# Performance work log

Measured on AMD Instinct MI355X. Metric: run time of the kernel, lower is better.

## Reference

```python
import jax, jax.numpy as jnp
import numpy as np

B, S, H = 2, 2048, 768
NH, DH = 12, 64  # num_heads, dim_head; inner_dim = NH*DH = H
SCALE = DH ** -0.5


def setup_inputs() -> dict:
    key = jax.random.key(0)
    k1, k2, k3 = jax.random.split(key, 3)
    x = jax.random.normal(k1, (B, S, H), dtype=jnp.float32)
    w_qkv = jax.random.normal(k2, (3 * NH * DH, H), dtype=jnp.float32) * (H ** -0.5)
    w_out = jax.random.normal(k3, (H, NH * DH), dtype=jnp.float32) * ((NH * DH) ** -0.5)
    b_out = jnp.zeros((H,), dtype=jnp.float32)
    return {"x": x, "w_qkv": w_qkv, "w_out": w_out, "b_out": b_out}


def reference(x, w_qkv, w_out, b_out):
    b, s, _ = x.shape
    # qkv linear: [b, s, 3*inner]
    qkv = jnp.einsum('bsh,oh->bso', x, w_qkv)
    # 'b s (qkv l d) -> qkv b l s d'  (l = heads)
    qkv = qkv.reshape(b, s, 3, NH, DH).transpose(2, 0, 3, 1, 4)
    q, k, v = qkv[0], qkv[1], qkv[2]  # each [b, nh, s, dh]
    att = jax.nn.softmax(jnp.einsum('bhxd,bhyd->bhxy', q, k) * SCALE, axis=-1)
    out = jnp.einsum('bhxy,bhyd->bhxd', att, v)  # [b, nh, s, dh]
    out = out.transpose(0, 2, 1, 3).reshape(b, s, NH * DH)  # 'b h l d -> b l (h d)'
    return jnp.einsum('bsi,oi->bso', out, w_out) + b_out
```

## Files before the change

### kernel.cpp

```cpp
#include <hip/hip_runtime.h>
#include <cstdint>
#include <cstddef>

typedef __bf16 bf16;
typedef __bf16 bf16x8 __attribute__((ext_vector_type(8)));
typedef __bf16 bf16x4 __attribute__((ext_vector_type(4)));
typedef float  f32x4  __attribute__((ext_vector_type(4)));
typedef float  f32x16 __attribute__((ext_vector_type(16)));

constexpr int Bb  = 2;
constexpr int Ss  = 2048;
constexpr int Hh  = 768;
constexpr int NHh = 12;
constexpr int DHh = 64;
constexpr int Mm  = Bb * Ss;
constexpr int N3  = 3 * Hh;
constexpr int QKW = 2 * Hh;

__device__ __forceinline__ float fexp2(float x) { return __builtin_amdgcn_exp2f(x); }

__device__ __forceinline__ void gload_lds16(void* lds, const void* g) {
  __builtin_amdgcn_global_load_lds(
      (__attribute__((address_space(1))) void*)(uintptr_t)g,
      (__attribute__((address_space(3))) void*)(uint32_t)(uintptr_t)lds,
      16, 0, 0);
}

__device__ __forceinline__ void cfence() { asm volatile("" ::: "memory"); }

__global__ void cvt3_f32_bf16(const float* __restrict__ x,  bf16* __restrict__ xb,
                              const float* __restrict__ w1, bf16* __restrict__ w1b,
                              const float* __restrict__ w2, bf16* __restrict__ w2b) {
  const int st = gridDim.x * blockDim.x;
  int i0 = blockIdx.x * blockDim.x + threadIdx.x;
  for (int i = i0; i < 786432; i += st) {
    float4 v = ((const float4*)x)[i];
    bf16x4 o; o[0]=(bf16)v.x; o[1]=(bf16)v.y; o[2]=(bf16)v.z; o[3]=(bf16)v.w;
    ((bf16x4*)xb)[i] = o;
  }
  for (int i = i0; i < 442368; i += st) {
    float4 v = ((const float4*)w1)[i];
    bf16x4 o; o[0]=(bf16)v.x; o[1]=(bf16)v.y; o[2]=(bf16)v.z; o[3]=(bf16)v.w;
    ((bf16x4*)w1b)[i] = o;
  }
  for (int i = i0; i < 147456; i += st) {
    float4 v = ((const float4*)w2)[i];
    bf16x4 o; o[0]=(bf16)v.x; o[1]=(bf16)v.y; o[2]=(bf16)v.z; o[3]=(bf16)v.w;
    ((bf16x4*)w2b)[i] = o;
  }
}

template<int CSTRIDE, int OUTMODE, int BM>
__global__ __launch_bounds__(256, 2)
void gemm_bt(const bf16* __restrict__ A, const bf16* __restrict__ Bw,
             bf16* __restrict__ Cb, bf16* __restrict__ VtG,
             float* __restrict__ Cf, const float* __restrict__ bias)
{
  constexpr int K = 768;
  constexpr int NT = K / 32;
  constexpr int MI = BM / 32;
  constexpr int ABUF = BM * 64;
  __shared__ bf16 As[2][BM * 32];
  __shared__ bf16 Bs[2][128 * 32];
  const int tid  = threadIdx.x;
  const int wid  = tid >> 6, lane = tid & 63;
  const int lr   = lane & 15, lk = lane >> 4;
  const int n0   = blockIdx.x * 128, m0 = blockIdx.y * BM;
  const int wm   = (wid >> 1) * (BM / 2), wn = (wid & 1) * 64;

  f32x4 acc[MI][4] = {};

  const char* Ag = (const char*)(A  + (size_t)m0 * K) + (size_t)(tid >> 2) * (K * 2) + (tid & 3) * 16;
  const char* Bg = (const char*)(Bw + (size_t)n0 * K) + (size_t)(tid >> 2) * (K * 2) + (tid & 3) * 16;
  constexpr size_t rstep = (size_t)64 * K * 2;

  auto stage = [&](int buf, int kb) {
    char* aw = (char*)As + buf * ABUF + wid * 1024;
    char* bw = (char*)Bs + buf * 8192 + wid * 1024;
    gload_lds16(aw, Ag + (size_t)kb * 2);
    if constexpr (BM == 128)
      gload_lds16(aw + 4096, Ag + rstep + (size_t)kb * 2);
    gload_lds16(bw,        Bg + (size_t)kb * 2);
    gload_lds16(bw + 4096, Bg + rstep + (size_t)kb * 2);
  };

  stage(0, 0);
  asm volatile("s_waitcnt vmcnt(0)" ::: "memory");
  __syncthreads();

#pragma unroll 1
  for (int t = 0; t < NT; ++t) {
    const int cur = t & 1;
    if (t + 1 < NT) stage(cur ^ 1, (t + 1) * 32);
    __builtin_amdgcn_sched_barrier(0);

    bf16x8 af[MI], bfv[4];
#pragma unroll
    for (int i = 0; i < MI; ++i)
      af[i]  = *(const bf16x8*)((const char*)As + cur * ABUF + ((wm + i * 16 + lr) * 32 + lk * 8) * 2);
#pragma unroll
    for (int j = 0; j < 4; ++j)
      bfv[j] = *(const bf16x8*)((const char*)Bs + cur * 8192 + ((wn + j * 16 + lr) * 32 + lk * 8) * 2);
#pragma unroll
    for (int i = 0; i < MI; ++i)
#pragma unroll
      for (int j = 0; j < 4; ++j)
        acc[i][j] = __builtin_amdgcn_mfma_f32_16x16x32_bf16(af[i], bfv[j], acc[i][j], 0, 0, 0);

    __syncthreads();
  }

  if constexpr (OUTMODE == 1) {
#pragma unroll
    for (int i = 0; i < MI; ++i)
#pragma unroll
      for (int j = 0; j < 4; ++j) {
        const int n = n0 + wn + j * 16 + lr;
        const float bv = bias[n];
#pragma unroll
        for (int r = 0; r < 4; ++r) {
          const int m = m0 + wm + i * 16 + lk * 4 + r;
          Cf[(size_t)m * CSTRIDE + n] = acc[i][j][r] + bv;
        }
      }
  } else {
    if (n0 < QKW) {
#pragma unroll
      for (int i = 0; i < MI; ++i)
#pragma unroll
        for (int j = 0; j < 4; ++j) {
          const int n = n0 + wn + j * 16 + lr;
#pragma unroll
          for (int r = 0; r < 4; ++r) {
            const int m = m0 + wm + i * 16 + lk * 4 + r;
            Cb[(size_t)m * CSTRIDE + n] = (bf16)acc[i][j][r];
          }
        }
    } else {
      const int bidx = m0 >> 11;
      const int s0 = (m0 & 2047) + wm + lk * 4;
#pragma unroll
      for (int i = 0; i < MI; ++i)
#pragma unroll
        for (int j = 0; j < 4; ++j) {
          const int colv = (n0 - QKW) + wn + j * 16 + lr;
          const int hh = colv >> 6, dd = colv & 63;
          const int bh = bidx * NHh + hh;
          const int mb = s0 + i * 16;
          bf16x4 pv;
#pragma unroll
          for (int r = 0; r < 4; ++r) pv[r] = (bf16)acc[i][j][r];
          const size_t idx8 = (((size_t)bh * 128 + (mb >> 4)) * 2 + (dd >> 5)) * 64
                              + ((mb >> 3) & 1) * 32 + (dd & 31);
          *(bf16x4*)(VtG + idx8 * 8 + (mb & 7)) = pv;
        }
    }
  }
}

__global__ __launch_bounds__(256, 3)
void attn_fwd5(const bf16* __restrict__ qk, const bf16* __restrict__ Vfrag,
               bf16* __restrict__ aout)
{
  __shared__ __align__(16) char lds[32768];
  const int tid  = threadIdx.x;
  const int wid  = tid >> 6, lane = tid & 63;
  const int lq   = lane & 31, hi = lane >> 5;
  const int qh   = wid & 1, grp = wid >> 1;

  const int orig = blockIdx.x;
  const int swz  = (orig & 7) * 96 + (orig >> 3);
  const int qb   = swz & 31;
  const int bh   = swz >> 5;
  const int b    = bh / NHh, h = bh % NHh;
  const int q0   = qb * 64 + qh * 32;
  const int kvbase = grp * 1024;

  constexpr float Cs = 0.18033688011112042f;
  const bf16* qrow = qk + (size_t)(b * Ss + q0 + lq) * QKW + h * DHh;
  bf16x8 qf[4];
#pragma unroll
  for (int j = 0; j < 4; ++j) {
    bf16x8 t = *(const bf16x8*)(qrow + j * 16 + hi * 8);
#pragma unroll
    for (int e = 0; e < 8; ++e) t[e] = (bf16)((float)t[e] * Cs);
    qf[j] = t;
  }

  const int strow = qh * 32 + (lane >> 3);
  const int stcol = ((lane & 7) * 16) ^ (((lane >> 3) & 7) << 4);
  const char* Kg0 = (const char*)(qk + (size_t)(b * Ss) * QKW + Hh + h * DHh)
                    + (size_t)strow * (QKW * 2) + stcol;
  auto stageK = [&](int buf, int kvt) {
    char* db = lds + grp * 16384 + buf * 8192 + qh * 4096;
    const char* sg = Kg0 + (size_t)kvt * (QKW * 2);
#pragma unroll
    for (int c = 0; c < 4; ++c)
      gload_lds16(db + c * 1024, sg + (size_t)(c * 8) * (QKW * 2));
  };

  const char* Vf = (const char*)Vfrag + (size_t)bh * 262144 + lane * 16;

  f32x16 oacc[2] = {};
  f32x16 lacc = {};
  bf16x8 ones;
#pragma unroll
  for (int e = 0; e < 8; ++e) ones[e] = (bf16)1.0f;

  stageK(0, kvbase);
  asm volatile("s_waitcnt vmcnt(0)" ::: "memory");
  __builtin_amdgcn_sched_barrier(0);

#pragma unroll 1
  for (int i = 0; i < 16; ++i) {
    const int cur = i & 1;

    cfence();
    __builtin_amdgcn_s_barrier();
    cfence();

    bf16x8 vf[4][2];
    {
      const char* vp = Vf + (size_t)(grp * 64 + i * 4) * 2048;
#pragma unroll
      for (int s = 0; s < 4; ++s)
#pragma unroll
        for (int dc = 0; dc < 2; ++dc)
          vf[s][dc] = *(const bf16x8*)(vp + (s * 2 + dc) * 1024);
    }

    stageK(cur ^ 1, kvbase + ((i + 1) & 15) * 64);
    __builtin_amdgcn_sched_barrier(0);

    f32x16 sacc[2];
    __builtin_amdgcn_s_setprio(1);
#pragma unroll
    for (int kvc = 0; kvc < 2; ++kvc) {
      f32x16 s = {};
      const int row = kvc * 32 + lq;
      const char* kb = lds + grp * 16384 + cur * 8192 + row * 128;
      const int sw = (lq & 7) << 4;
#pragma unroll
      for (int j = 0; j < 4; ++j) {
        bf16x8 kf = *(const bf16x8*)(kb + ((j * 32 + hi * 16) ^ sw));
        s = __builtin_amdgcn_mfma_f32_32x32x16_bf16(kf, qf[j], s, 0, 0, 0);
      }
      sacc[kvc] = s;
    }
    __builtin_amdgcn_s_setprio(0);

    uint32_t w[2][8];
#pragma unroll
    for (int kvc = 0; kvc < 2; ++kvc)
#pragma unroll
      for (int m = 0; m < 8; ++m) {
        union { bf16 hh[2]; uint32_t u; } cv;
        cv.hh[0] = (bf16)fexp2(sacc[kvc][2 * m]);
        cv.hh[1] = (bf16)fexp2(sacc[kvc][2 * m + 1]);
        w[kvc][m] = cv.u;
      }

    asm volatile("s_waitcnt vmcnt(4)" ::: "memory");
    __builtin_amdgcn_sched_barrier(0);

    __builtin_amdgcn_s_setprio(1);
#pragma unroll
    for (int s = 0; s < 4; ++s) {
      const int kvc = s >> 1, sb = s & 1;
      uint32_t a0 = w[kvc][4 * sb + 0], b0 = w[kvc][4 * sb + 2];
      uint32_t a1 = w[kvc][4 * sb + 1], b1 = w[kvc][4 * sb + 3];
      asm("v_permlane32_swap_b32 %0, %1" : "+v"(a0), "+v"(b0));
      asm("v_permlane32_swap_b32 %0, %1" : "+v"(a1), "+v"(b1));
      union { uint32_t u[4]; bf16x8 v; } pf;
      pf.u[0] = a0; pf.u[1] = a1; pf.u[2] = b0; pf.u[3] = b1;
#pragma unroll
      for (int dc = 0; dc < 2; ++dc)
        oacc[dc] = __builtin_amdgcn_mfma_f32_32x32x16_bf16(vf[s][dc], pf.v, oacc[dc], 0, 0, 0);
      lacc = __builtin_amdgcn_mfma_f32_32x32x16_bf16(ones, pf.v, lacc, 0, 0, 0);
    }
    __builtin_amdgcn_s_setprio(0);

    asm volatile("s_waitcnt vmcnt(0)" ::: "memory");
    __builtin_amdgcn_sched_barrier(0);
  }

  __syncthreads();

  if (grp == 1) {
    char* mb = lds + qh * 8704;
#pragma unroll
    for (int dc = 0; dc < 2; ++dc)
#pragma unroll
      for (int rr = 0; rr < 4; ++rr) {
        f32x4 t;
#pragma unroll
        for (int e = 0; e < 4; ++e) t[e] = oacc[dc][rr * 4 + e];
        *(f32x4*)(mb + (dc * 4 + rr) * 1024 + lane * 16) = t;
      }
    *(float*)(mb + 8192 + lane * 4) = lacc[0];
  }
  __syncthreads();
  if (grp == 0) {
    const char* mb = lds + qh * 8704;
    const float l2 = *(const float*)(mb + 8192 + lane * 4);
    const float linv = 1.0f / (lacc[0] + l2);
    bf16* orow = aout + (size_t)(b * Ss + q0 + lq) * Hh + h * DHh;
#pragma unroll
    for (int dc = 0; dc < 2; ++dc)
#pragma unroll
      for (int rr = 0; rr < 4; ++rr) {
        const f32x4 o2 = *(const f32x4*)(mb + (dc * 4 + rr) * 1024 + lane * 16);
        bf16x4 ov;
#pragma unroll
        for (int e = 0; e < 4; ++e)
          ov[e] = (bf16)((oacc[dc][rr * 4 + e] + o2[e]) * linv);
        *(bf16x4*)(orow + dc * 32 + rr * 8 + hi * 4) = ov;
      }
  }
}

extern "C" void kernel_launch(void* const* d_in, const int* in_sizes, int n_in,
                              void* d_out, int out_size, void* d_ws, size_t ws_size,
                              hipStream_t stream) {
  const float* x     = (const float*)d_in[0];
  const float* w_qkv = (const float*)d_in[1];
  const float* w_out = (const float*)d_in[2];
  const float* b_out = (const float*)d_in[3];
  char* ws = (char*)d_ws;
  bf16* xb    = (bf16*)(ws + 0);
  bf16* wqkvb = (bf16*)(ws + 6291456);
  bf16* woutb = (bf16*)(ws + 9830400);
  bf16* qkb   = (bf16*)(ws + 11010048);
  bf16* Vfrag = (bf16*)(ws + 23592960);
  bf16* aoutb = (bf16*)(ws + 29884416);

  cvt3_f32_bf16<<<2048, 256, 0, stream>>>(x, xb, w_qkv, wqkvb, w_out, woutb);

  gemm_bt<QKW, 0, 128><<<dim3(18, 32), 256, 0, stream>>>(xb, wqkvb, qkb, Vfrag, nullptr, nullptr);
  attn_fwd5<<<768, 256, 0, stream>>>(qkb, Vfrag, aoutb);
  gemm_bt<Hh, 1, 64><<<dim3(6, 64), 256, 0, stream>>>(aoutb, woutb, nullptr, nullptr,
                                                      (float*)d_out, b_out);
}
```

Before: 87.76 us.

## Write K in MFMA fragment layout from QKV GEMM for contiguous attention staging

The QKV projection epilogue now writes Q to its own row-major buffer and writes K directly in a per-head, MFMA-fragment-ordered layout, as was already done for V. The attention kernel then stages K tiles with fully contiguous 16-byte global-to-LDS loads and reads them from LDS without the XOR swizzle. The intended gains are coalesced K loads and conflict-free LDS reads in the attention loop. The cost is scattered 2-byte scalar stores in the GEMM epilogue for K, which may slow the projection kernel.

```diff
diff --git a/kernel.cpp b/kernel.cpp
--- a/kernel.cpp
+++ b/kernel.cpp
@@ -50,10 +50,10 @@
   }
 }
 
-template<int CSTRIDE, int OUTMODE, int BM>
+template<int OUTMODE, int BM>
 __global__ __launch_bounds__(256, 2)
 void gemm_bt(const bf16* __restrict__ A, const bf16* __restrict__ Bw,
-             bf16* __restrict__ Cb, bf16* __restrict__ VtG,
+             bf16* __restrict__ Qb, bf16* __restrict__ Kf, bf16* __restrict__ Vf,
              float* __restrict__ Cf, const float* __restrict__ bias)
 {
   constexpr int K = 768;
@@ -120,11 +120,13 @@
 #pragma unroll
         for (int r = 0; r < 4; ++r) {
           const int m = m0 + wm + i * 16 + lk * 4 + r;
-          Cf[(size_t)m * CSTRIDE + n] = acc[i][j][r] + bv;
+          Cf[(size_t)m * Hh + n] = acc[i][j][r] + bv;
         }
       }
   } else {
-    if (n0 < QKW) {
+    const int bidx = m0 >> 11;
+    const int kvb  = (m0 & 2047) + wm + lk * 4;
+    if (n0 < Hh) {
 #pragma unroll
       for (int i = 0; i < MI; ++i)
 #pragma unroll
@@ -133,12 +135,26 @@
 #pragma unroll
           for (int r = 0; r < 4; ++r) {
             const int m = m0 + wm + i * 16 + lk * 4 + r;
-            Cb[(size_t)m * CSTRIDE + n] = (bf16)acc[i][j][r];
+            Qb[(size_t)m * Hh + n] = (bf16)acc[i][j][r];
+          }
+        }
+    } else if (n0 < QKW) {
+#pragma unroll
+      for (int i = 0; i < MI; ++i)
+#pragma unroll
+        for (int j = 0; j < 4; ++j) {
+          const int colv = (n0 - Hh) + wn + j * 16 + lr;
+          const int hh = colv >> 6, dd = colv & 63;
+          bf16* kfh = Kf + (size_t)(bidx * NHh + hh) * 131072;
+#pragma unroll
+          for (int r = 0; r < 4; ++r) {
+            const int kv = kvb + i * 16 + r;
+            const size_t idx = (size_t)((((kv >> 5) * 4 + (dd >> 4)) * 64
+                                + ((dd >> 3) & 1) * 32 + (kv & 31)) * 8 + (dd & 7));
+            kfh[idx] = (bf16)acc[i][j][r];
           }
         }
     } else {
-      const int bidx = m0 >> 11;
-      const int s0 = (m0 & 2047) + wm + lk * 4;
 #pragma unroll
       for (int i = 0; i < MI; ++i)
 #pragma unroll
@@ -146,21 +162,21 @@
           const int colv = (n0 - QKW) + wn + j * 16 + lr;
           const int hh = colv >> 6, dd = colv & 63;
           const int bh = bidx * NHh + hh;
-          const int mb = s0 + i * 16;
+          const int mb = kvb + i * 16;
           bf16x4 pv;
 #pragma unroll
           for (int r = 0; r < 4; ++r) pv[r] = (bf16)acc[i][j][r];
           const size_t idx8 = (((size_t)bh * 128 + (mb >> 4)) * 2 + (dd >> 5)) * 64
                               + ((mb >> 3) & 1) * 32 + (dd & 31);
-          *(bf16x4*)(VtG + idx8 * 8 + (mb & 7)) = pv;
+          *(bf16x4*)(Vf + idx8 * 8 + (mb & 7)) = pv;
         }
     }
   }
 }
 
 __global__ __launch_bounds__(256, 3)
-void attn_fwd5(const bf16* __restrict__ qk, const bf16* __restrict__ Vfrag,
-               bf16* __restrict__ aout)
+void attn_fwd10(const bf16* __restrict__ Qb, const bf16* __restrict__ Kfrag,
+                const bf16* __restrict__ Vfrag, bf16* __restrict__ aout)
 {
   __shared__ __align__(16) char lds[32768];
   const int tid  = threadIdx.x;
@@ -174,10 +190,9 @@
   const int bh   = swz >> 5;
   const int b    = bh / NHh, h = bh % NHh;
   const int q0   = qb * 64 + qh * 32;
-  const int kvbase = grp * 1024;
 
   constexpr float Cs = 0.18033688011112042f;
-  const bf16* qrow = qk + (size_t)(b * Ss + q0 + lq) * QKW + h * DHh;
+  const bf16* qrow = Qb + (size_t)(b * Ss + q0 + lq) * Hh + h * DHh;
   bf16x8 qf[4];
 #pragma unroll
   for (int j = 0; j < 4; ++j) {
@@ -187,19 +202,16 @@
     qf[j] = t;
   }
 
-  const int strow = qh * 32 + (lane >> 3);
-  const int stcol = ((lane & 7) * 16) ^ (((lane >> 3) & 7) << 4);
-  const char* Kg0 = (const char*)(qk + (size_t)(b * Ss) * QKW + Hh + h * DHh)
-                    + (size_t)strow * (QKW * 2) + stcol;
-  auto stageK = [&](int buf, int kvt) {
+  const char* Kfg = (const char*)Kfrag + (size_t)bh * 262144 + grp * 131072 + lane * 16;
+  auto stageK = [&](int buf, int it) {
     char* db = lds + grp * 16384 + buf * 8192 + qh * 4096;
-    const char* sg = Kg0 + (size_t)kvt * (QKW * 2);
+    const char* sg = Kfg + (size_t)it * 8192 + qh * 4096;
 #pragma unroll
     for (int c = 0; c < 4; ++c)
-      gload_lds16(db + c * 1024, sg + (size_t)(c * 8) * (QKW * 2));
+      gload_lds16(db + c * 1024, sg + c * 1024);
   };
 
-  const char* Vf = (const char*)Vfrag + (size_t)bh * 262144 + lane * 16;
+  const char* Vfp = (const char*)Vfrag + (size_t)bh * 262144 + grp * 131072 + lane * 16;
 
   f32x16 oacc[2] = {};
   f32x16 lacc = {};
@@ -207,7 +219,7 @@
 #pragma unroll
   for (int e = 0; e < 8; ++e) ones[e] = (bf16)1.0f;
 
-  stageK(0, kvbase);
+  stageK(0, 0);
   asm volatile("s_waitcnt vmcnt(0)" ::: "memory");
   __builtin_amdgcn_sched_barrier(0);
 
@@ -221,7 +233,7 @@
 
     bf16x8 vf[4][2];
     {
-      const char* vp = Vf + (size_t)(grp * 64 + i * 4) * 2048;
+      const char* vp = Vfp + (size_t)i * 8192;
 #pragma unroll
       for (int s = 0; s < 4; ++s)
 #pragma unroll
@@ -229,7 +241,7 @@
           vf[s][dc] = *(const bf16x8*)(vp + (s * 2 + dc) * 1024);
     }
 
-    stageK(cur ^ 1, kvbase + ((i + 1) & 15) * 64);
+    stageK(cur ^ 1, (i + 1) & 15);
     __builtin_amdgcn_sched_barrier(0);
 
     f32x16 sacc[2];
@@ -237,12 +249,10 @@
 #pragma unroll
     for (int kvc = 0; kvc < 2; ++kvc) {
       f32x16 s = {};
-      const int row = kvc * 32 + lq;
-      const char* kb = lds + grp * 16384 + cur * 8192 + row * 128;
-      const int sw = (lq & 7) << 4;
+      const char* kb = lds + grp * 16384 + cur * 8192 + kvc * 4096 + lane * 16;
 #pragma unroll
       for (int j = 0; j < 4; ++j) {
-        bf16x8 kf = *(const bf16x8*)(kb + ((j * 32 + hi * 16) ^ sw));
+        bf16x8 kf = *(const bf16x8*)(kb + j * 1024);
         s = __builtin_amdgcn_mfma_f32_32x32x16_bf16(kf, qf[j], s, 0, 0, 0);
       }
       sacc[kvc] = s;
@@ -330,14 +340,16 @@
   bf16* xb    = (bf16*)(ws + 0);
   bf16* wqkvb = (bf16*)(ws + 6291456);
   bf16* woutb = (bf16*)(ws + 9830400);
-  bf16* qkb   = (bf16*)(ws + 11010048);
+  bf16* Qb    = (bf16*)(ws + 11010048);
+  bf16* Kfrag = (bf16*)(ws + 17301504);
   bf16* Vfrag = (bf16*)(ws + 23592960);
   bf16* aoutb = (bf16*)(ws + 29884416);
 
   cvt3_f32_bf16<<<2048, 256, 0, stream>>>(x, xb, w_qkv, wqkvb, w_out, woutb);
 
-  gemm_bt<QKW, 0, 128><<<dim3(18, 32), 256, 0, stream>>>(xb, wqkvb, qkb, Vfrag, nullptr, nullptr);
-  attn_fwd5<<<768, 256, 0, stream>>>(qkb, Vfrag, aoutb);
-  gemm_bt<Hh, 1, 64><<<dim3(6, 64), 256, 0, stream>>>(aoutb, woutb, nullptr, nullptr,
-                                                      (float*)d_out, b_out);
-}
+  gemm_bt<0, 128><<<dim3(18, 32), 256, 0, stream>>>(xb, wqkvb, Qb, Kfrag, Vfrag,
+                                                    nullptr, nullptr);
+  attn_fwd10<<<768, 256, 0, stream>>>(Qb, Kfrag, Vfrag, aoutb);
+  gemm_bt<1, 64><<<dim3(6, 64), 256, 0, stream>>>(aoutb, woutb, nullptr, nullptr, nullptr,
+                                                  (float*)d_out, b_out);
+}
```

Result: no change. 87.92 us (+0.2%).
